# Optimization experiments

Measured on AMD Instinct MI355X. Metric: run time of the kernel, lower is better.

## Reference

```python
import jax, jax.numpy as jnp
import numpy as np

B, C, K, H, W = 8, 256, 19, 256, 256  # batch, input_nc, num_classes, spatial
NEG_SLOPE = 0.2


def setup_inputs() -> dict:
    key = jax.random.key(0)
    ks = jax.random.split(key, 12)
    x = jax.random.normal(ks[0], (B, C, H, W), jnp.float32)
    cam = jax.random.uniform(ks[1], (B, K, H, W), jnp.float32)
    gt = jax.random.randint(ks[2], (B, K), 0, 3, jnp.int32)
    gt_src = jax.random.uniform(ks[3], (B, K, K), jnp.float32)
    gt_tgt = jax.random.uniform(ks[4], (B, K, K), jnp.float32)
    weights = jax.random.uniform(ks[5], (B, K), jnp.float32)
    W1 = jax.random.normal(ks[6], (C, 2048), jnp.float32) * 0.02
    b1 = jnp.zeros((2048,), jnp.float32)
    W2 = jax.random.normal(ks[7], (2048, 512), jnp.float32) * 0.02
    b2 = jnp.zeros((512,), jnp.float32)
    Wc = jax.random.normal(ks[8], (512, 2 * K), jnp.float32) * 0.02
    bc = jnp.zeros((2 * K,), jnp.float32)
    return {"x": x, "cam": cam, "gt": gt, "gt_src": gt_src, "gt_tgt": gt_tgt,
            "weights": weights, "W1": W1, "b1": b1, "W2": W2, "b2": b2,
            "Wc": Wc, "bc": bc}


def reference(x, cam, gt, gt_src, gt_tgt, weights, W1, b1, W2, b2, Wc, bc):
    hw = x.shape[-1] * x.shape[-2]
    # cams_feature: mean over HW of cam[:,:,None]*x[:,None] -> [B, K, C]
    feat = jnp.einsum('bkhw,bchw->bkc', cam, x) / hw
    # Small MLP (self.D) + cls head, batched over all B*K rows; masking
    # replaces the per-sample ragged gather (extra rows are masked out below).
    h = jax.nn.leaky_relu(feat @ W1 + b1, NEG_SLOPE)
    h = jax.nn.leaky_relu(h @ W2 + b2, NEG_SLOPE)
    logits = h @ Wc + bc                      # [B, K, 2K]
    mask = (gt > 0).astype(logits.dtype)      # [B, K] selected rows
    lbl = jnp.concatenate([gt_src, gt_tgt], axis=-1)  # [B, K, 2K]
    logp = jax.nn.log_softmax(logits, axis=-1)
    ce = -(lbl * logp).sum(-1)                # [B, K]
    n = mask.sum(-1)                          # rows per sample
    sample_loss = (mask * weights * ce).sum(-1) / jnp.maximum(n, 1.0)
    lbl_sum = (mask[..., None] * lbl).sum((-2, -1))   # per-sample label mass
    valid = lbl_sum > 0                       # skip samples with lbl.sum()==0
    batch_size = x.shape[0]
    loss_img = jnp.where(valid, sample_loss, 0.0).sum() / batch_size
    match = (jnp.argmax(logits, -1) == jnp.argmax(lbl, -1)).astype(logits.dtype) * mask
    acc = jnp.where(valid, match.sum(-1), 0.0).sum()
    cnt = jnp.where(valid, lbl_sum, 0.0).sum()
    acc_img = acc / cnt * 100.0
    return jnp.stack([loss_img, acc_img])
```

## Files before the change

### kernel.cpp

```cpp
#include <hip/hip_runtime.h>
#include <stdint.h>

#define BB 8
#define CC 256
#define KK 19
#define HWN 65536
#define H1 2048
#define H2 512
#define NC 38
#define NEG 0.2f
#define NSL 16
#define HWS (HWN / NSL)
#define HWT 256
#define NCH (HWS / HWT)
#define CAMF4 (KK * HWT / 4)
#define NROW (BB * KK)

__device__ __forceinline__ void gload_lds16(const float4* g, float4* l) {
    __builtin_amdgcn_global_load_lds(
        (const __attribute__((address_space(1))) void*)g,
        (__attribute__((address_space(3))) void*)l, 16, 0, 0);
}

__global__ __launch_bounds__(256) void k_feat(const float* __restrict__ x,
                                              const float* __restrict__ cam,
                                              float* __restrict__ partial) {
    __shared__ float cams[2][KK * HWT];
    const int b  = blockIdx.y;
    const int cg = blockIdx.x & 15;
    const int sl = blockIdx.x >> 4;
    const int t  = threadIdx.x;
    const int w  = t >> 6;
    const int l  = t & 63;
    const int c0 = cg * 16 + w * 4;

    const float4* __restrict__ x4  = reinterpret_cast<const float4*>(x);
    const float4* __restrict__ cb4 = reinterpret_cast<const float4*>(cam) + (size_t)b * KK * (HWN / 4);
    const int slbase = sl * (HWS / 4);

    float acc[KK][4];
#pragma unroll
    for (int k = 0; k < KK; ++k)
#pragma unroll
        for (int c = 0; c < 4; ++c) acc[k][c] = 0.f;

    auto stage = [&](int buf, int ch) {
        const int f0 = slbase + ch * (HWT / 4);
#pragma unroll
        for (int j = 0; j < 5; ++j) {
            const int idx = w * 64 + j * 256;
            if (idx < CAMF4) {
                const int row = idx >> 6;
                gload_lds16(cb4 + (size_t)row * (HWN / 4) + f0 + l,
                            ((float4*)cams[buf]) + idx + l);
            }
        }
    };
    auto loadx = [&](float4 (&xv)[4], int ch) {
        const int f0 = slbase + ch * (HWT / 4);
#pragma unroll
        for (int c = 0; c < 4; ++c)
            xv[c] = x4[(size_t)(b * CC + c0 + c) * (HWN / 4) + f0 + l];
    };
    auto consume = [&](int buf, const float4 (&xv)[4]) {
        const float4* cs = (const float4*)cams[buf];
#pragma unroll
        for (int k = 0; k < KK; ++k) {
            const float4 cv = cs[k * (HWT / 4) + l];
#pragma unroll
            for (int c = 0; c < 4; ++c)
                acc[k][c] = fmaf(xv[c].w, cv.w, fmaf(xv[c].z, cv.z,
                            fmaf(xv[c].y, cv.y, fmaf(xv[c].x, cv.x, acc[k][c]))));
        }
    };

    float4 xa[4], xb[4];
    loadx(xa, 0);
    stage(0, 0);
    __syncthreads();

#pragma unroll 1
    for (int ch = 0; ch < NCH; ch += 2) {
        loadx(xb, ch + 1);
        stage(1, ch + 1);
        consume(0, xa);
        __syncthreads();
        if (ch + 2 < NCH) { loadx(xa, ch + 2); stage(0, ch + 2); }
        consume(1, xb);
        __syncthreads();
    }

#pragma unroll
    for (int k = 0; k < KK; ++k) {
#pragma unroll
        for (int c = 0; c < 4; ++c) {
            float v = acc[k][c];
#pragma unroll
            for (int off = 32; off; off >>= 1) v += __shfl_xor(v, off, 64);
            if (l == 0)
                partial[(size_t)sl * (NROW * CC) +
                        (size_t)(b * KK + k) * CC + c0 + c] = v;
        }
    }
}

__global__ __launch_bounds__(256) void k_mlp1(const float* __restrict__ partial,
                                              const float* __restrict__ W1,
                                              const float* __restrict__ b1,
                                              float* __restrict__ h1,
                                              float* __restrict__ scal) {
    __shared__ float fr[2][CC];
    const int r0 = blockIdx.y * 2;
    const int t  = threadIdx.x;
    if (blockIdx.x == 0 && blockIdx.y == 0 && t < 16) scal[t] = 0.f;

    float s0 = 0.f, s1 = 0.f;
#pragma unroll
    for (int slc = 0; slc < NSL; ++slc) {
        s0 += partial[((size_t)slc * NROW + r0) * CC + t];
        s1 += partial[((size_t)slc * NROW + r0 + 1) * CC + t];
    }
    fr[0][t] = s0 * (1.0f / (float)HWN);
    fr[1][t] = s1 * (1.0f / (float)HWN);
    __syncthreads();

    const int j = blockIdx.x * 256 + t;
    const float4* f0 = (const float4*)fr[0];
    const float4* f1 = (const float4*)fr[1];
    const float bias = b1[j];
    float a0 = bias, a1 = bias;
#pragma unroll 8
    for (int c4 = 0; c4 < CC / 4; ++c4) {
        const float4 v0 = f0[c4], v1 = f1[c4];
        const size_t cb = (size_t)(c4 * 4) * H1 + j;
        const float w0 = W1[cb], w1 = W1[cb + H1], w2 = W1[cb + 2 * H1], w3 = W1[cb + 3 * H1];
        a0 = fmaf(v0.x, w0, a0); a0 = fmaf(v0.y, w1, a0); a0 = fmaf(v0.z, w2, a0); a0 = fmaf(v0.w, w3, a0);
        a1 = fmaf(v1.x, w0, a1); a1 = fmaf(v1.y, w1, a1); a1 = fmaf(v1.z, w2, a1); a1 = fmaf(v1.w, w3, a1);
    }
    h1[(size_t)r0 * H1 + j]       = a0 > 0.f ? a0 : NEG * a0;
    h1[(size_t)(r0 + 1) * H1 + j] = a1 > 0.f ? a1 : NEG * a1;
}

__global__ __launch_bounds__(128) void k_mlp2p(const float* __restrict__ h1,
                                               const float* __restrict__ W2,
                                               float* __restrict__ part) {
    const int j  = blockIdx.x * 128 + threadIdx.x;
    const int r0 = blockIdx.y * 2;
    const int cb = blockIdx.z * 512;
    const float4* __restrict__ f0 = reinterpret_cast<const float4*>(h1 + (size_t)r0 * H1 + cb);
    const float4* __restrict__ f1 = reinterpret_cast<const float4*>(h1 + (size_t)(r0 + 1) * H1 + cb);

    float a0 = 0.f, a1 = 0.f;
#pragma unroll 8
    for (int c4 = 0; c4 < 128; ++c4) {
        const float4 v0 = f0[c4], v1 = f1[c4];
        const size_t wb = (size_t)(cb + c4 * 4) * H2 + j;
        const float w0 = W2[wb], w1 = W2[wb + H2], w2 = W2[wb + 2 * H2], w3 = W2[wb + 3 * H2];
        a0 = fmaf(v0.x, w0, a0); a0 = fmaf(v0.y, w1, a0); a0 = fmaf(v0.z, w2, a0); a0 = fmaf(v0.w, w3, a0);
        a1 = fmaf(v1.x, w0, a1); a1 = fmaf(v1.y, w1, a1); a1 = fmaf(v1.z, w2, a1); a1 = fmaf(v1.w, w3, a1);
    }
    part[((size_t)blockIdx.z * NROW + r0) * H2 + j]     = a0;
    part[((size_t)blockIdx.z * NROW + r0 + 1) * H2 + j] = a1;
}

__global__ __launch_bounds__(768) void k_loss(const float* __restrict__ part,
                                              const float* __restrict__ b2,
                                              const float* __restrict__ Wc,
                                              const float* __restrict__ bc,
                                              const int* __restrict__ gt,
                                              const float* __restrict__ gt_src,
                                              const float* __restrict__ gt_tgt,
                                              const float* __restrict__ wts,
                                              float* __restrict__ scal) {
    __shared__ float h2s[KK][H2];
    __shared__ float lg[KK][NC];
    __shared__ float rloss[KK], rmask[KK], rlbl[KK], rmatch[KK];

    const int b = blockIdx.x;
    const int t = threadIdx.x;

    for (int i = t; i < KK * H2; i += 768) {
        const int row = b * KK + (i >> 9);
        const int jj  = i & 511;
        float s = b2[jj];
#pragma unroll
        for (int p = 0; p < 4; ++p)
            s += part[((size_t)p * NROW + row) * H2 + jj];
        ((float*)h2s)[i] = s > 0.f ? s : NEG * s;
    }
    __syncthreads();

    if (t < KK * NC) {
        const int k = t / NC, j = t % NC;
        float acc = bc[j];
        for (int c = 0; c < H2; ++c) acc = fmaf(h2s[k][c], Wc[(size_t)c * NC + j], acc);
        lg[k][j] = acc;
    }
    __syncthreads();

    if (t < KK) {
        const int k = t;
        float m = -1e30f; int am = 0;
        for (int j = 0; j < NC; ++j) {
            float v = lg[k][j];
            if (v > m) { m = v; am = j; }
        }
        float se = 0.f, celbl = 0.f, lsum = 0.f, lm = -1e30f; int al = 0;
        for (int j = 0; j < NC; ++j) {
            float v = lg[k][j];
            se += expf(v - m);
            float lb = (j < KK) ? gt_src[((size_t)b * KK + k) * KK + j]
                                : gt_tgt[((size_t)b * KK + k) * KK + (j - KK)];
            celbl = fmaf(lb, v, celbl);
            lsum += lb;
            if (lb > lm) { lm = lb; al = j; }
        }
        float lse = m + logf(se);
        float ce = lse * lsum - celbl;
        float mask = (gt[b * KK + k] > 0) ? 1.f : 0.f;
        rloss[k]  = mask * wts[b * KK + k] * ce;
        rmask[k]  = mask;
        rlbl[k]   = mask * lsum;
        rmatch[k] = mask * ((am == al) ? 1.f : 0.f);
    }
    __syncthreads();

    if (t == 0) {
        float n = 0.f, sl = 0.f, ls = 0.f, mt = 0.f;
        for (int k = 0; k < KK; ++k) { n += rmask[k]; sl += rloss[k]; ls += rlbl[k]; mt += rmatch[k]; }
        float sample_loss = sl / fmaxf(n, 1.f);
        bool valid = ls > 0.f;
        atomicAdd(&scal[0], valid ? sample_loss : 0.f);
        atomicAdd(&scal[1], valid ? mt : 0.f);
        atomicAdd(&scal[2], valid ? ls : 0.f);
    }
}

__global__ void k_final(const float* __restrict__ scal, float* __restrict__ out) {
    out[0] = scal[0] / (float)BB;
    out[1] = scal[1] / scal[2] * 100.f;
}

extern "C" void kernel_launch(void* const* d_in, const int* in_sizes, int n_in,
                              void* d_out, int out_size, void* d_ws, size_t ws_size,
                              hipStream_t stream) {
    const float* x      = (const float*)d_in[0];
    const float* cam    = (const float*)d_in[1];
    const int*   gt     = (const int*)d_in[2];
    const float* gt_src = (const float*)d_in[3];
    const float* gt_tgt = (const float*)d_in[4];
    const float* wts    = (const float*)d_in[5];
    const float* W1     = (const float*)d_in[6];
    const float* b1     = (const float*)d_in[7];
    const float* W2     = (const float*)d_in[8];
    const float* b2     = (const float*)d_in[9];
    const float* Wc     = (const float*)d_in[10];
    const float* bc     = (const float*)d_in[11];

    float* ws      = (float*)d_ws;
    float* scal    = ws;
    float* partial = ws + 16;
    float* h1      = partial + (size_t)NSL * NROW * CC;
    float* part2   = h1 + (size_t)NROW * H1;

    dim3 g1(16 * NSL, BB);
    k_feat<<<g1, 256, 0, stream>>>(x, cam, partial);
    dim3 g2(H1 / 256, NROW / 2);
    k_mlp1<<<g2, 256, 0, stream>>>(partial, W1, b1, h1, scal);
    dim3 g3(4, NROW / 2, 4);
    k_mlp2p<<<g3, 128, 0, stream>>>(h1, W2, part2);
    k_loss<<<BB, 768, 0, stream>>>(part2, b2, Wc, bc, gt, gt_src, gt_tgt, wts, scal);
    k_final<<<1, 1, 0, stream>>>(scal, (float*)d_out);
}
```

Before: 270.9 us.

## Drop LDS staging of cam; read cam directly from global per wave

Removes the double-buffered global_load_lds staging of the cam tile into shared memory along with the block barriers. Each wave now loads x and cam straight from global memory in a simple loop with no software pipelining. This avoids LDS traffic and __syncthreads, and the lower LDS use may allow more resident blocks. In exchange, the four waves of a block each fetch the same cam data, relying on the L1/L2 caches, and there is no explicit prefetch to hide load latency.

After: 617.8 us. 2.28x slower.

```diff
diff --git a/kernel.cpp b/kernel.cpp
--- a/kernel.cpp
+++ b/kernel.cpp
@@ -13,19 +13,11 @@
 #define HWS (HWN / NSL)
 #define HWT 256
 #define NCH (HWS / HWT)
-#define CAMF4 (KK * HWT / 4)
 #define NROW (BB * KK)
-
-__device__ __forceinline__ void gload_lds16(const float4* g, float4* l) {
-    __builtin_amdgcn_global_load_lds(
-        (const __attribute__((address_space(1))) void*)g,
-        (__attribute__((address_space(3))) void*)l, 16, 0, 0);
-}
 
 __global__ __launch_bounds__(256) void k_feat(const float* __restrict__ x,
                                               const float* __restrict__ cam,
                                               float* __restrict__ partial) {
-    __shared__ float cams[2][KK * HWT];
     const int b  = blockIdx.y;
     const int cg = blockIdx.x & 15;
     const int sl = blockIdx.x >> 4;
@@ -44,50 +36,23 @@
 #pragma unroll
         for (int c = 0; c < 4; ++c) acc[k][c] = 0.f;
 
-    auto stage = [&](int buf, int ch) {
-        const int f0 = slbase + ch * (HWT / 4);
-#pragma unroll
-        for (int j = 0; j < 5; ++j) {
-            const int idx = w * 64 + j * 256;
-            if (idx < CAMF4) {
-                const int row = idx >> 6;
-                gload_lds16(cb4 + (size_t)row * (HWN / 4) + f0 + l,
-                            ((float4*)cams[buf]) + idx + l);
-            }
-        }
-    };
-    auto loadx = [&](float4 (&xv)[4], int ch) {
-        const int f0 = slbase + ch * (HWT / 4);
+#pragma unroll 1
+    for (int ch = 0; ch < NCH; ++ch) {
+        const int f0 = slbase + ch * (HWT / 4) + l;
+
+        float4 xv[4];
 #pragma unroll
         for (int c = 0; c < 4; ++c)
-            xv[c] = x4[(size_t)(b * CC + c0 + c) * (HWN / 4) + f0 + l];
-    };
-    auto consume = [&](int buf, const float4 (&xv)[4]) {
-        const float4* cs = (const float4*)cams[buf];
+            xv[c] = x4[(size_t)(b * CC + c0 + c) * (HWN / 4) + f0];
+
 #pragma unroll
         for (int k = 0; k < KK; ++k) {
-            const float4 cv = cs[k * (HWT / 4) + l];
+            const float4 cv = cb4[(size_t)k * (HWN / 4) + f0];
 #pragma unroll
             for (int c = 0; c < 4; ++c)
                 acc[k][c] = fmaf(xv[c].w, cv.w, fmaf(xv[c].z, cv.z,
                             fmaf(xv[c].y, cv.y, fmaf(xv[c].x, cv.x, acc[k][c]))));
         }
-    };
-
-    float4 xa[4], xb[4];
-    loadx(xa, 0);
-    stage(0, 0);
-    __syncthreads();
-
-#pragma unroll 1
-    for (int ch = 0; ch < NCH; ch += 2) {
-        loadx(xb, ch + 1);
-        stage(1, ch + 1);
-        consume(0, xa);
-        __syncthreads();
-        if (ch + 2 < NCH) { loadx(xa, ch + 2); stage(0, ch + 2); }
-        consume(1, xb);
-        __syncthreads();
     }
 
 #pragma unroll
```
